# Kernel tuning notes

Hardware: AMD Instinct MI355X
Metric: run time of the kernel (lower is better)

The kernel has to match this reference:

```python
import jax, jax.numpy as jnp
import numpy as np

D_MODEL = 1024
N_HEADS = 16
HEAD_DIM = D_MODEL // N_HEADS
CHUNK = 128
B, T = 2, 2048


def setup_inputs() -> dict:
    key = jax.random.key(0)
    ks = jax.random.split(key, 5)
    x = jax.random.normal(ks[0], (B, T, D_MODEL), dtype=jnp.float32)
    mk = lambda k: jax.random.normal(k, (D_MODEL, D_MODEL), dtype=jnp.float32) * 0.02
    return {"x": x, "Wq": mk(ks[1]), "Wk": mk(ks[2]), "Wv": mk(ks[3]), "Wo": mk(ks[4])}


def _chunked_causal_attention(q, k, v, cs):
    # q,k,v: [B,H,T,D] fp32. Streaming online-softmax over kv chunks (flash-attn style).
    Bq, H, Tq, D = q.shape
    n = Tq // cs  # T divisible by chunk_size
    inv_sqrt_d = 1.0 / (D ** 0.5)
    qc = jnp.moveaxis(q.reshape(Bq, H, n, cs, D), 2, 0)  # [n,B,H,cs,D]
    kc = jnp.moveaxis(k.reshape(Bq, H, n, cs, D), 2, 0)
    vc = jnp.moveaxis(v.reshape(Bq, H, n, cs, D), 2, 0)
    ar = jnp.arange(cs)

    def per_q(qi, qb):  # qb: [B,H,cs,D]
        q_idx = qi * cs + ar

        def step(carry, kv):
            m, l, o = carry
            ki, kb, vb = kv
            s = jnp.einsum('bhqd,bhkd->bhqk', qb, kb) * inv_sqrt_d
            k_idx = ki * cs + ar
            causal = q_idx[:, None] >= k_idx[None, :]
            s = jnp.where(causal, s, -jnp.inf)
            s_max = jnp.max(s, axis=-1, keepdims=True)
            m_new = jnp.maximum(m, s_max)
            # guard fully-masked chunks (m_new = -inf)
            m_safe = jnp.where(jnp.isneginf(m_new), 0.0, m_new)
            alpha = jnp.exp(m - m_safe)
            p = jnp.exp(s - m_safe)
            o = o * alpha + jnp.einsum('bhqk,bhkd->bhqd', p, vb)
            l = l * alpha + jnp.sum(p, axis=-1, keepdims=True)
            return (m_new, l, o), None

        init = (jnp.full((Bq, H, cs, 1), -jnp.inf, dtype=jnp.float32),
                jnp.zeros((Bq, H, cs, 1), dtype=jnp.float32),
                jnp.zeros_like(qb))
        (m, l, o), _ = jax.lax.scan(step, init, (jnp.arange(n), kc, vc))
        return o / jnp.maximum(l, 1e-9)

    out = jax.vmap(per_q)(jnp.arange(n), qc)  # [n,B,H,cs,D]
    return jnp.moveaxis(out, 0, 2).reshape(Bq, H, Tq, D)


def reference(x, Wq, Wk, Wv, Wo):
    Bx, Tx, C = x.shape
    def heads(w):
        return (x @ w.T).reshape(Bx, Tx, N_HEADS, HEAD_DIM).transpose(0, 2, 1, 3)
    q, k, v = heads(Wq), heads(Wk), heads(Wv)
    y = _chunked_causal_attention(q, k, v, CHUNK)  # [B,H,T,D]
    y = y.transpose(0, 2, 1, 3).reshape(Bx, Tx, C)
    return y @ Wo.T
```

## Files before the change

### kernel.cpp

```cpp
#include <hip/hip_runtime.h>
#include <hip/hip_bf16.h>
#include <stdint.h>

typedef __bf16 bf16;
typedef __bf16 bf16x8 __attribute__((ext_vector_type(8)));
typedef __bf16 bf16x4 __attribute__((ext_vector_type(4)));
typedef float  f32x4  __attribute__((ext_vector_type(4)));

#define DM 1024
#define NH 16
#define HD 64
#define TT 2048

#define QSCALE 0.18033688011112042f

__global__ void cvt_all(const float* __restrict__ x,  const float* __restrict__ wq,
                        const float* __restrict__ wk, const float* __restrict__ wv,
                        const float* __restrict__ wo,
                        bf16* __restrict__ xb,  bf16* __restrict__ wqb,
                        bf16* __restrict__ wkb, bf16* __restrict__ wvb,
                        bf16* __restrict__ wob) {
  const int i = (blockIdx.x * blockDim.x + threadIdx.x) * 4;
  const float* src; bf16* dst; int off;
  if (i < 4194304)      { src = x;  dst = xb;  off = i; }
  else {
    const int j = i - 4194304;
    const int w = j >> 20;
    off = j & 1048575;
    src = (w == 0) ? wq : (w == 1) ? wk : (w == 2) ? wv : wo;
    dst = (w == 0) ? wqb : (w == 1) ? wkb : (w == 2) ? wvb : wob;
  }
  const float4 v = *reinterpret_cast<const float4*>(src + off);
  bf16x4 o = { (bf16)v.x, (bf16)v.y, (bf16)v.z, (bf16)v.w };
  *reinterpret_cast<bf16x4*>(dst + off) = o;
}

static __device__ __forceinline__ void gload_lds16(const bf16* g, bf16* l) {
  __builtin_amdgcn_global_load_lds(
      (__attribute__((address_space(1))) void*)g,
      (__attribute__((address_space(3))) void*)l, 16, 0, 0);
}

static __device__ __forceinline__ int swzb(int lin) {
  return lin ^ (((lin >> 7) & 7) << 4);
}

__launch_bounds__(256, 3)
__global__ void gemm_qkv(const bf16* __restrict__ X, const bf16* __restrict__ Wq,
                         const bf16* __restrict__ Wk, const bf16* __restrict__ Wv,
                         bf16* __restrict__ Qb, bf16* __restrict__ Kb,
                         bf16* __restrict__ Vtb) {
  __shared__ bf16 As[128 * 32];
  __shared__ bf16 Bs[128 * 32];
  const int tid  = threadIdx.x;
  const int lane = tid & 63;
  const int wv   = tid >> 6;
  const int lg   = lane >> 4, lc = lane & 15;
  const int m0   = blockIdx.x * 128;
  const int ng   = blockIdx.y * 128;
  const int which = ng >> 10;
  const bf16* W = (which == 0) ? Wq : ((which == 1) ? Wk : Wv);
  const int n0 = ng & 1023;
  const int wm = wv >> 1, wn = wv & 1;

  f32x4 acc[4][4] = {};

  for (int k0 = 0; k0 < DM; k0 += 32) {
#pragma unroll
    for (int c = 0; c < 2; ++c) {
      const int e   = wv * 512 + c * 2048 + lane * 8;
      const int row = e >> 5, col = e & 31;
      gload_lds16(X + (size_t)(m0 + row) * DM + k0 + col, &As[wv * 512 + c * 2048]);
      gload_lds16(W + (size_t)(n0 + row) * DM + k0 + col, &Bs[wv * 512 + c * 2048]);
    }
    __syncthreads();
    bf16x8 a[4], b[4];
#pragma unroll
    for (int i = 0; i < 4; ++i)
      a[i] = *reinterpret_cast<const bf16x8*>(&As[(wm * 64 + i * 16 + lc) * 32 + lg * 8]);
#pragma unroll
    for (int j = 0; j < 4; ++j)
      b[j] = *reinterpret_cast<const bf16x8*>(&Bs[(wn * 64 + j * 16 + lc) * 32 + lg * 8]);
#pragma unroll
    for (int i = 0; i < 4; ++i)
#pragma unroll
      for (int j = 0; j < 4; ++j)
        acc[i][j] = __builtin_amdgcn_mfma_f32_16x16x32_bf16(a[i], b[j], acc[i][j], 0, 0, 0);
    __syncthreads();
  }

#pragma unroll
  for (int i = 0; i < 4; ++i) {
    const int mg = m0 + wm * 64 + i * 16 + lg * 4;
    const int bb = mg >> 11, t = mg & 2047;
#pragma unroll
    for (int j = 0; j < 4; ++j) {
      const int nl = n0 + wn * 64 + j * 16 + lc;
      const int h = nl >> 6, d = nl & 63;
      const int bh = bb * NH + h;
      const f32x4 v = acc[i][j];
      if (which == 0) {
        bf16* p = Qb + ((size_t)bh * TT + t) * HD + d;
#pragma unroll
        for (int r = 0; r < 4; ++r) p[r * HD] = (bf16)(v[r] * QSCALE);
      } else if (which == 1) {
        bf16* p = Kb + ((size_t)bh * TT + t) * HD + d;
#pragma unroll
        for (int r = 0; r < 4; ++r) p[r * HD] = (bf16)v[r];
      } else {
        bf16x4 pk = { (bf16)v[0], (bf16)v[1], (bf16)v[2], (bf16)v[3] };
        *reinterpret_cast<bf16x4*>(Vtb + ((size_t)bh * HD + d) * TT + t) = pk;
      }
    }
  }
}

#define KPAD 72

__launch_bounds__(512, 2)
__global__ void attn_fwd(const bf16* __restrict__ Qb, const bf16* __restrict__ Kb,
                         const bf16* __restrict__ Vtb, bf16* __restrict__ Yb) {
  __shared__ bf16 Ks[2][4096];
  __shared__ bf16 Vs[2][4096];
  __shared__ bf16 Ps[8][16 * KPAD];

  const int tid  = threadIdx.x;
  const int lane = tid & 63;
  const int wv   = tid >> 6;
  const int lg   = lane >> 4;
  const int lc   = lane & 15;
  const int bh   = blockIdx.x & 31;
  const int pr   = blockIdx.x >> 5;
  const int qblkA = 8 + pr, qblkB = 7 - pr;
  const int nt0  = 2 * qblkA + 2;

  const bf16* Qg = Qb  + (size_t)bh * TT * HD;
  const bf16* Kg = Kb  + (size_t)bh * TT * HD;
  const bf16* Vg = Vtb + (size_t)bh * HD * TT;

  bf16x8 qA0, qA1, qB0, qB1;
  qA0 = *reinterpret_cast<const bf16x8*>(Qg + (size_t)(qblkA * 128 + wv * 16 + lc) * HD + 0  + lg * 8);
  qA1 = *reinterpret_cast<const bf16x8*>(Qg + (size_t)(qblkA * 128 + wv * 16 + lc) * HD + 32 + lg * 8);
  qB0 = *reinterpret_cast<const bf16x8*>(Qg + (size_t)(qblkB * 128 + wv * 16 + lc) * HD + 0  + lg * 8);
  qB1 = *reinterpret_cast<const bf16x8*>(Qg + (size_t)(qblkB * 128 + wv * 16 + lc) * HD + 32 + lg * 8);

  const int lin  = tid * 16;
  const int dstb = wv * 1024;
  const int koff = swzb(lin);
  const int voff = (lin >> 7) * (TT * 2) + (swzb(lin) & 127);

  auto STAGE = [&](int b, int kv) {
    gload_lds16((const bf16*)((const char*)Kg + (size_t)kv * 8192 + koff),
                (bf16*)((char*)Ks[b] + dstb));
    gload_lds16((const bf16*)((const char*)Vg + (size_t)kv * 128 + voff),
                (bf16*)((char*)Vs[b] + dstb));
  };

  f32x4 o[4] = {};
  float m_run = -INFINITY, l_run = 0.f;
  int   q0 = qblkA * 128;
  bf16x8 qf0 = qA0, qf1 = qA1;
  bf16* Pw = Ps[wv];
  const int b_ = bh >> 4, h_ = bh & 15;

  STAGE(0, 0);
  __syncthreads();

  int cur = 0;
  for (int ti = 0; ti < 34; ++ti) {
    const int kv = (ti < nt0) ? ti : ti - nt0;
    const int k0 = kv * 64;

    if (ti + 1 < 34) {
      const int tn = ti + 1;
      STAGE(cur ^ 1, (tn < nt0) ? tn : tn - nt0);
    }

    const char* ksb = (const char*)Ks[cur];
    const char* vsb = (const char*)Vs[cur];

    f32x4 s[4] = {};
#pragma unroll
    for (int kvf = 0; kvf < 4; ++kvf) {
      const bf16x8 k0f = *reinterpret_cast<const bf16x8*>(
          ksb + swzb((kvf * 16 + lc) * 128 + lg * 16));
      s[kvf] = __builtin_amdgcn_mfma_f32_16x16x32_bf16(k0f, qf0, s[kvf], 0, 0, 0);
      const bf16x8 k1f = *reinterpret_cast<const bf16x8*>(
          ksb + swzb((kvf * 16 + lc) * 128 + 64 + lg * 16));
      s[kvf] = __builtin_amdgcn_mfma_f32_16x16x32_bf16(k1f, qf1, s[kvf], 0, 0, 0);
    }

    const int qw = q0 + wv * 16;
    if (k0 + 63 > qw) {
      const int q = qw + lc;
#pragma unroll
      for (int kvf = 0; kvf < 4; ++kvf)
#pragma unroll
        for (int r = 0; r < 4; ++r)
          if (k0 + kvf * 16 + lg * 4 + r > q) s[kvf][r] = -INFINITY;
    }

    float rmax = -INFINITY;
#pragma unroll
    for (int kvf = 0; kvf < 4; ++kvf)
#pragma unroll
      for (int r = 0; r < 4; ++r) rmax = fmaxf(rmax, s[kvf][r]);
    rmax = fmaxf(rmax, __shfl_xor(rmax, 16));
    rmax = fmaxf(rmax, __shfl_xor(rmax, 32));

    const float mn = fmaxf(m_run, rmax);
    const float alpha = __builtin_amdgcn_exp2f(m_run - mn);
    m_run = mn;

    float rsum = 0.f;
#pragma unroll
    for (int kvf = 0; kvf < 4; ++kvf)
#pragma unroll
      for (int r = 0; r < 4; ++r) {
        const float p = __builtin_amdgcn_exp2f(s[kvf][r] - mn);
        s[kvf][r] = p;
        rsum += p;
      }
    rsum += __shfl_xor(rsum, 16);
    rsum += __shfl_xor(rsum, 32);
    l_run = l_run * alpha + rsum;

#pragma unroll
    for (int df = 0; df < 4; ++df)
#pragma unroll
      for (int r = 0; r < 4; ++r) o[df][r] *= alpha;

#pragma unroll
    for (int kvf = 0; kvf < 4; ++kvf) {
      bf16x4 pk = { (bf16)s[kvf][0], (bf16)s[kvf][1],
                    (bf16)s[kvf][2], (bf16)s[kvf][3] };
      *reinterpret_cast<bf16x4*>(&Pw[lc * KPAD + kvf * 16 + lg * 4]) = pk;
    }

#pragma unroll
    for (int ks = 0; ks < 2; ++ks) {
      const bf16x8 pf = *reinterpret_cast<const bf16x8*>(
          &Pw[lc * KPAD + ks * 32 + lg * 8]);
#pragma unroll
      for (int df = 0; df < 4; ++df) {
        const bf16x8 vf = *reinterpret_cast<const bf16x8*>(
            vsb + swzb((df * 16 + lc) * 128 + ks * 64 + lg * 16));
        o[df] = __builtin_amdgcn_mfma_f32_16x16x32_bf16(vf, pf, o[df], 0, 0, 0);
      }
    }

    if (ti == nt0 - 1) {
      const float linv = 1.f / fmaxf(l_run, 1e-9f);
      const int q = q0 + wv * 16 + lc;
#pragma unroll
      for (int df = 0; df < 4; ++df) {
        bf16x4 yv = { (bf16)(o[df][0] * linv), (bf16)(o[df][1] * linv),
                      (bf16)(o[df][2] * linv), (bf16)(o[df][3] * linv) };
        *reinterpret_cast<bf16x4*>(
            Yb + ((size_t)(b_ * TT + q)) * DM + h_ * HD + df * 16 + lg * 4) = yv;
        o[df] = f32x4{};
      }
      m_run = -INFINITY; l_run = 0.f;
      q0 = qblkB * 128;
      qf0 = qB0; qf1 = qB1;
    }

    __syncthreads();
    cur ^= 1;
  }

  {
    const float linv = 1.f / fmaxf(l_run, 1e-9f);
    const int q = q0 + wv * 16 + lc;
#pragma unroll
    for (int df = 0; df < 4; ++df) {
      bf16x4 yv = { (bf16)(o[df][0] * linv), (bf16)(o[df][1] * linv),
                    (bf16)(o[df][2] * linv), (bf16)(o[df][3] * linv) };
      *reinterpret_cast<bf16x4*>(
          Yb + ((size_t)(b_ * TT + q)) * DM + h_ * HD + df * 16 + lg * 4) = yv;
    }
  }
}

__launch_bounds__(256, 2)
__global__ void gemm_out(const bf16* __restrict__ Y, const bf16* __restrict__ Wo,
                         float* __restrict__ Out) {
  __shared__ bf16 As[128 * 32];
  __shared__ bf16 Bs[128 * 32];
  const int tid  = threadIdx.x;
  const int lane = tid & 63;
  const int wv   = tid >> 6;
  const int lg   = lane >> 4, lc = lane & 15;
  const int m0   = blockIdx.x * 128;
  const int n0   = blockIdx.y * 128;
  const int wm = wv >> 1, wn = wv & 1;

  f32x4 acc[4][4] = {};

  for (int k0 = 0; k0 < DM; k0 += 32) {
#pragma unroll
    for (int c = 0; c < 2; ++c) {
      const int e   = wv * 512 + c * 2048 + lane * 8;
      const int row = e >> 5, col = e & 31;
      gload_lds16(Y  + (size_t)(m0 + row) * DM + k0 + col, &As[wv * 512 + c * 2048]);
      gload_lds16(Wo + (size_t)(n0 + row) * DM + k0 + col, &Bs[wv * 512 + c * 2048]);
    }
    __syncthreads();
    bf16x8 a[4], b[4];
#pragma unroll
    for (int i = 0; i < 4; ++i)
      a[i] = *reinterpret_cast<const bf16x8*>(&As[(wm * 64 + i * 16 + lc) * 32 + lg * 8]);
#pragma unroll
    for (int j = 0; j < 4; ++j)
      b[j] = *reinterpret_cast<const bf16x8*>(&Bs[(wn * 64 + j * 16 + lc) * 32 + lg * 8]);
#pragma unroll
    for (int i = 0; i < 4; ++i)
#pragma unroll
      for (int j = 0; j < 4; ++j)
        acc[i][j] = __builtin_amdgcn_mfma_f32_16x16x32_bf16(a[i], b[j], acc[i][j], 0, 0, 0);
    __syncthreads();
  }

#pragma unroll
  for (int i = 0; i < 4; ++i) {
    const int mg = m0 + wm * 64 + i * 16 + lg * 4;
#pragma unroll
    for (int j = 0; j < 4; ++j) {
      const int n = n0 + wn * 64 + j * 16 + lc;
#pragma unroll
      for (int r = 0; r < 4; ++r)
        Out[(size_t)(mg + r) * DM + n] = acc[i][j][r];
    }
  }
}

extern "C" void kernel_launch(void* const* d_in, const int* in_sizes, int n_in,
                              void* d_out, int out_size, void* d_ws, size_t ws_size,
                              hipStream_t stream) {
  const float* x  = (const float*)d_in[0];
  const float* Wq = (const float*)d_in[1];
  const float* Wk = (const float*)d_in[2];
  const float* Wv = (const float*)d_in[3];
  const float* Wo = (const float*)d_in[4];
  float* out = (float*)d_out;
  char* ws = (char*)d_ws;
  const size_t MB = 1024 * 1024;

  bf16* xb  = (bf16*)(ws + 0);
  bf16* wqb = (bf16*)(ws + 8  * MB);
  bf16* wkb = (bf16*)(ws + 10 * MB);
  bf16* wvb = (bf16*)(ws + 12 * MB);
  bf16* wob = (bf16*)(ws + 14 * MB);
  bf16* Qb  = (bf16*)(ws + 16 * MB);
  bf16* Kb  = (bf16*)(ws + 24 * MB);
  bf16* Vtb = (bf16*)(ws + 32 * MB);
  bf16* yb  = xb;

  cvt_all<<<8192, 256, 0, stream>>>(x, Wq, Wk, Wv, Wo, xb, wqb, wkb, wvb, wob);
  gemm_qkv<<<dim3(32, 24), 256, 0, stream>>>(xb, wqb, wkb, wvb, Qb, Kb, Vtb);
  attn_fwd<<<256, 512, 0, stream>>>(Qb, Kb, Vtb, yb);
  gemm_out<<<dim3(32, 8), 256, 0, stream>>>(yb, wob, out);
}
```

Measured before the change: 114.3 us.

## Halve attention and out-proj tiles for more blocks, add explicit waitcnt pipelining

The attention kernel moves from 512-thread blocks over 128-row query tiles to 256-thread blocks over 64-row query tiles, still pairing a late and an early tile for causal balance, which doubles the grid to 512 blocks. The prefetch wait becomes an explicit vmcnt wait plus a raw barrier, and s_setprio is raised around the MFMA sections. The output GEMM tile is halved in M to 64, doubling its grid. The aim is better CU occupancy and load balance on the many-CU part, at the cost of less K/V reuse per block and a larger total number of tile loads.

```diff
diff --git a/kernel.cpp b/kernel.cpp
--- a/kernel.cpp
+++ b/kernel.cpp
@@ -117,12 +117,12 @@
 
 #define KPAD 72
 
-__launch_bounds__(512, 2)
+__launch_bounds__(256, 2)
 __global__ void attn_fwd(const bf16* __restrict__ Qb, const bf16* __restrict__ Kb,
                          const bf16* __restrict__ Vtb, bf16* __restrict__ Yb) {
   __shared__ bf16 Ks[2][4096];
   __shared__ bf16 Vs[2][4096];
-  __shared__ bf16 Ps[8][16 * KPAD];
+  __shared__ bf16 Ps[4][16 * KPAD];
 
   const int tid  = threadIdx.x;
   const int lane = tid & 63;
@@ -131,55 +131,69 @@
   const int lc   = lane & 15;
   const int bh   = blockIdx.x & 31;
   const int pr   = blockIdx.x >> 5;
-  const int qblkA = 8 + pr, qblkB = 7 - pr;
-  const int nt0  = 2 * qblkA + 2;
+  const int qblkA = 16 + pr, qblkB = 15 - pr;
+  const int nt0  = qblkA + 1;
+  const int NT   = 33;
 
   const bf16* Qg = Qb  + (size_t)bh * TT * HD;
   const bf16* Kg = Kb  + (size_t)bh * TT * HD;
   const bf16* Vg = Vtb + (size_t)bh * HD * TT;
 
   bf16x8 qA0, qA1, qB0, qB1;
-  qA0 = *reinterpret_cast<const bf16x8*>(Qg + (size_t)(qblkA * 128 + wv * 16 + lc) * HD + 0  + lg * 8);
-  qA1 = *reinterpret_cast<const bf16x8*>(Qg + (size_t)(qblkA * 128 + wv * 16 + lc) * HD + 32 + lg * 8);
-  qB0 = *reinterpret_cast<const bf16x8*>(Qg + (size_t)(qblkB * 128 + wv * 16 + lc) * HD + 0  + lg * 8);
-  qB1 = *reinterpret_cast<const bf16x8*>(Qg + (size_t)(qblkB * 128 + wv * 16 + lc) * HD + 32 + lg * 8);
-
-  const int lin  = tid * 16;
-  const int dstb = wv * 1024;
-  const int koff = swzb(lin);
-  const int voff = (lin >> 7) * (TT * 2) + (swzb(lin) & 127);
+  qA0 = *reinterpret_cast<const bf16x8*>(Qg + (size_t)(qblkA * 64 + wv * 16 + lc) * HD + 0  + lg * 8);
+  qA1 = *reinterpret_cast<const bf16x8*>(Qg + (size_t)(qblkA * 64 + wv * 16 + lc) * HD + 32 + lg * 8);
+  qB0 = *reinterpret_cast<const bf16x8*>(Qg + (size_t)(qblkB * 64 + wv * 16 + lc) * HD + 0  + lg * 8);
+  qB1 = *reinterpret_cast<const bf16x8*>(Qg + (size_t)(qblkB * 64 + wv * 16 + lc) * HD + 32 + lg * 8);
+
+  int dstb[2], koff[2], voff[2];
+#pragma unroll
+  for (int c = 0; c < 2; ++c) {
+    const int base = (wv * 2 + c) * 1024;
+    const int lin  = base + lane * 16;
+    dstb[c] = base;
+    koff[c] = swzb(lin);
+    voff[c] = (lin >> 7) * (TT * 2) + (swzb(lin) & 127);
+  }
 
   auto STAGE = [&](int b, int kv) {
-    gload_lds16((const bf16*)((const char*)Kg + (size_t)kv * 8192 + koff),
-                (bf16*)((char*)Ks[b] + dstb));
-    gload_lds16((const bf16*)((const char*)Vg + (size_t)kv * 128 + voff),
-                (bf16*)((char*)Vs[b] + dstb));
+#pragma unroll
+    for (int c = 0; c < 2; ++c) {
+      gload_lds16((const bf16*)((const char*)Kg + (size_t)kv * 8192 + koff[c]),
+                  (bf16*)((char*)Ks[b] + dstb[c]));
+      gload_lds16((const bf16*)((const char*)Vg + (size_t)kv * 128 + voff[c]),
+                  (bf16*)((char*)Vs[b] + dstb[c]));
+    }
   };
 
   f32x4 o[4] = {};
   float m_run = -INFINITY, l_run = 0.f;
-  int   q0 = qblkA * 128;
+  int   q0 = qblkA * 64;
   bf16x8 qf0 = qA0, qf1 = qA1;
   bf16* Pw = Ps[wv];
   const int b_ = bh >> 4, h_ = bh & 15;
 
   STAGE(0, 0);
-  __syncthreads();
 
   int cur = 0;
-  for (int ti = 0; ti < 34; ++ti) {
+  for (int ti = 0; ti < NT; ++ti) {
     const int kv = (ti < nt0) ? ti : ti - nt0;
     const int k0 = kv * 64;
 
-    if (ti + 1 < 34) {
+    if (ti + 1 < NT) {
       const int tn = ti + 1;
       STAGE(cur ^ 1, (tn < nt0) ? tn : tn - nt0);
-    }
+      asm volatile("s_waitcnt vmcnt(4)" ::: "memory");
+    } else {
+      asm volatile("s_waitcnt vmcnt(0)" ::: "memory");
+    }
+    __builtin_amdgcn_s_barrier();
+    __builtin_amdgcn_sched_barrier(0);
 
     const char* ksb = (const char*)Ks[cur];
     const char* vsb = (const char*)Vs[cur];
 
     f32x4 s[4] = {};
+    __builtin_amdgcn_s_setprio(1);
 #pragma unroll
     for (int kvf = 0; kvf < 4; ++kvf) {
       const bf16x8 k0f = *reinterpret_cast<const bf16x8*>(
@@ -189,6 +203,7 @@
           ksb + swzb((kvf * 16 + lc) * 128 + 64 + lg * 16));
       s[kvf] = __builtin_amdgcn_mfma_f32_16x16x32_bf16(k1f, qf1, s[kvf], 0, 0, 0);
     }
+    __builtin_amdgcn_s_setprio(0);
 
     const int qw = q0 + wv * 16;
     if (k0 + 63 > qw) {
@@ -200,11 +215,11 @@
           if (k0 + kvf * 16 + lg * 4 + r > q) s[kvf][r] = -INFINITY;
     }
 
-    float rmax = -INFINITY;
-#pragma unroll
-    for (int kvf = 0; kvf < 4; ++kvf)
-#pragma unroll
-      for (int r = 0; r < 4; ++r) rmax = fmaxf(rmax, s[kvf][r]);
+    float t0 = fmaxf(fmaxf(s[0][0], s[0][1]), fmaxf(s[0][2], s[0][3]));
+    float t1 = fmaxf(fmaxf(s[1][0], s[1][1]), fmaxf(s[1][2], s[1][3]));
+    float t2 = fmaxf(fmaxf(s[2][0], s[2][1]), fmaxf(s[2][2], s[2][3]));
+    float t3 = fmaxf(fmaxf(s[3][0], s[3][1]), fmaxf(s[3][2], s[3][3]));
+    float rmax = fmaxf(fmaxf(t0, t1), fmaxf(t2, t3));
     rmax = fmaxf(rmax, __shfl_xor(rmax, 16));
     rmax = fmaxf(rmax, __shfl_xor(rmax, 32));
 
@@ -212,15 +227,17 @@
     const float alpha = __builtin_amdgcn_exp2f(m_run - mn);
     m_run = mn;
 
-    float rsum = 0.f;
 #pragma unroll
     for (int kvf = 0; kvf < 4; ++kvf)
 #pragma unroll
-      for (int r = 0; r < 4; ++r) {
-        const float p = __builtin_amdgcn_exp2f(s[kvf][r] - mn);
-        s[kvf][r] = p;
-        rsum += p;
-      }
+      for (int r = 0; r < 4; ++r)
+        s[kvf][r] = __builtin_amdgcn_exp2f(s[kvf][r] - mn);
+
+    float u0 = (s[0][0] + s[0][1]) + (s[0][2] + s[0][3]);
+    float u1 = (s[1][0] + s[1][1]) + (s[1][2] + s[1][3]);
+    float u2 = (s[2][0] + s[2][1]) + (s[2][2] + s[2][3]);
+    float u3 = (s[3][0] + s[3][1]) + (s[3][2] + s[3][3]);
+    float rsum = (u0 + u1) + (u2 + u3);
     rsum += __shfl_xor(rsum, 16);
     rsum += __shfl_xor(rsum, 32);
     l_run = l_run * alpha + rsum;
@@ -237,6 +254,7 @@
       *reinterpret_cast<bf16x4*>(&Pw[lc * KPAD + kvf * 16 + lg * 4]) = pk;
     }
 
+    __builtin_amdgcn_s_setprio(1);
 #pragma unroll
     for (int ks = 0; ks < 2; ++ks) {
       const bf16x8 pf = *reinterpret_cast<const bf16x8*>(
@@ -248,6 +266,7 @@
         o[df] = __builtin_amdgcn_mfma_f32_16x16x32_bf16(vf, pf, o[df], 0, 0, 0);
       }
     }
+    __builtin_amdgcn_s_setprio(0);
 
     if (ti == nt0 - 1) {
       const float linv = 1.f / fmaxf(l_run, 1e-9f);
@@ -261,11 +280,11 @@
         o[df] = f32x4{};
       }
       m_run = -INFINITY; l_run = 0.f;
-      q0 = qblkB * 128;
+      q0 = qblkB * 64;
       qf0 = qB0; qf1 = qB1;
     }
 
-    __syncthreads();
+    __builtin_amdgcn_s_barrier();
     cur ^= 1;
   }
 
@@ -285,36 +304,40 @@
 __launch_bounds__(256, 2)
 __global__ void gemm_out(const bf16* __restrict__ Y, const bf16* __restrict__ Wo,
                          float* __restrict__ Out) {
-  __shared__ bf16 As[128 * 32];
+  __shared__ bf16 As[64 * 32];
   __shared__ bf16 Bs[128 * 32];
   const int tid  = threadIdx.x;
   const int lane = tid & 63;
   const int wv   = tid >> 6;
   const int lg   = lane >> 4, lc = lane & 15;
-  const int m0   = blockIdx.x * 128;
+  const int m0   = blockIdx.x * 64;
   const int n0   = blockIdx.y * 128;
   const int wm = wv >> 1, wn = wv & 1;
 
-  f32x4 acc[4][4] = {};
+  f32x4 acc[2][4] = {};
 
   for (int k0 = 0; k0 < DM; k0 += 32) {
+    {
+      const int e   = wv * 512 + lane * 8;
+      const int row = e >> 5, col = e & 31;
+      gload_lds16(Y + (size_t)(m0 + row) * DM + k0 + col, &As[wv * 512]);
+    }
 #pragma unroll
     for (int c = 0; c < 2; ++c) {
-      const int e   = wv * 512 + c * 2048 + lane * 8;
+      const int e   = wv * 1024 + c * 512 + lane * 8;
       const int row = e >> 5, col = e & 31;
-      gload_lds16(Y  + (size_t)(m0 + row) * DM + k0 + col, &As[wv * 512 + c * 2048]);
-      gload_lds16(Wo + (size_t)(n0 + row) * DM + k0 + col, &Bs[wv * 512 + c * 2048]);
+      gload_lds16(Wo + (size_t)(n0 + row) * DM + k0 + col, &Bs[wv * 1024 + c * 512]);
     }
     __syncthreads();
-    bf16x8 a[4], b[4];
-#pragma unroll
-    for (int i = 0; i < 4; ++i)
-      a[i] = *reinterpret_cast<const bf16x8*>(&As[(wm * 64 + i * 16 + lc) * 32 + lg * 8]);
+    bf16x8 a[2], b[4];
+#pragma unroll
+    for (int i = 0; i < 2; ++i)
+      a[i] = *reinterpret_cast<const bf16x8*>(&As[(wm * 32 + i * 16 + lc) * 32 + lg * 8]);
 #pragma unroll
     for (int j = 0; j < 4; ++j)
       b[j] = *reinterpret_cast<const bf16x8*>(&Bs[(wn * 64 + j * 16 + lc) * 32 + lg * 8]);
 #pragma unroll
-    for (int i = 0; i < 4; ++i)
+    for (int i = 0; i < 2; ++i)
 #pragma unroll
       for (int j = 0; j < 4; ++j)
         acc[i][j] = __builtin_amdgcn_mfma_f32_16x16x32_bf16(a[i], b[j], acc[i][j], 0, 0, 0);
@@ -322,8 +345,8 @@
   }
 
 #pragma unroll
-  for (int i = 0; i < 4; ++i) {
-    const int mg = m0 + wm * 64 + i * 16 + lg * 4;
+  for (int i = 0; i < 2; ++i) {
+    const int mg = m0 + wm * 32 + i * 16 + lg * 4;
 #pragma unroll
     for (int j = 0; j < 4; ++j) {
       const int n = n0 + wn * 64 + j * 16 + lc;
@@ -358,6 +381,6 @@
 
   cvt_all<<<8192, 256, 0, stream>>>(x, Wq, Wk, Wv, Wo, xb, wqb, wkb, wvb, wob);
   gemm_qkv<<<dim3(32, 24), 256, 0, stream>>>(xb, wqb, wkb, wvb, Qb, Kb, Vtb);
-  attn_fwd<<<256, 512, 0, stream>>>(Qb, Kb, Vtb, yb);
-  gemm_out<<<dim3(32, 8), 256, 0, stream>>>(yb, wob, out);
-}
+  attn_fwd<<<512, 256, 0, stream>>>(Qb, Kb, Vtb, yb);
+  gemm_out<<<dim3(64, 8), 256, 0, stream>>>(yb, wob, out);
+}
```

After: 110.7 us. 3.2% less time.
